# Performance work log

Measured on AMD Instinct MI355X. Metric: run time of the kernel, lower is better.

## Reference

```python
import jax, jax.numpy as jnp
import numpy as np

D_MODEL = 1024
N_HEADS = 16
D_HEAD = D_MODEL // N_HEADS

def setup_inputs() -> dict:
    key = jax.random.key(0)
    k1, k2, k3 = jax.random.split(key, 3)
    x = jax.random.normal(k1, (4, 2048, D_MODEL), dtype=jnp.float32)
    # Linear weights stored as [in, out] for x @ W
    s = 1.0 / np.sqrt(D_MODEL)
    W_qkv = jax.random.uniform(k2, (D_MODEL, 3 * D_MODEL), jnp.float32, -s, s)
    W_out = jax.random.uniform(k3, (D_MODEL, D_MODEL), jnp.float32, -s, s)
    return {"x": x, "W_qkv": W_qkv, "W_out": W_out}

def reference(x, W_qkv, W_out):
    B, T, C = x.shape
    scale = D_HEAD ** -0.5
    qkv = x @ W_qkv                       # [B,T,3C]
    q, k, v = jnp.split(qkv, 3, axis=-1)
    def heads(t):
        return t.reshape(B, T, N_HEADS, D_HEAD).transpose(0, 2, 1, 3)  # [B,H,T,d]
    q, k, v = heads(q), heads(k), heads(v)
    att = jnp.einsum('bhqd,bhkd->bhqk', q, k) * scale  # [B,H,T,T]
    causal = jnp.tril(jnp.ones((T, T), dtype=bool))
    att = jnp.where(causal, att, -jnp.inf)
    att = jax.nn.softmax(att, axis=-1)
    y = jnp.einsum('bhqk,bhkd->bhqd', att, v)          # [B,H,T,d]
    y = y.transpose(0, 2, 1, 3).reshape(B, T, C)
    return y @ W_out
```

## Files before the change

### kernel.cpp

```cpp
#include <hip/hip_runtime.h>
#include <hip/hip_bf16.h>

typedef unsigned short u16;
typedef __attribute__((ext_vector_type(8))) short short8v;
typedef __attribute__((ext_vector_type(4))) float f32x4;
typedef __attribute__((ext_vector_type(16))) float f32x16;

#define Bb 4
#define Tt 2048
#define Cc 1024
#define Hh 16
#define C3 3072
#define Mm 8192

__device__ __forceinline__ u16 f2bf(float f) {
    union { __hip_bfloat16 h; u16 u; } r;
    r.h = __float2bfloat16(f);
    return r.u;
}
__device__ __forceinline__ unsigned int pk2(float a, float b) {
    union { __hip_bfloat162 h; unsigned int u; } r;
    r.h.x = __float2bfloat16(a);
    r.h.y = __float2bfloat16(b);
    return r.u;
}
__device__ __forceinline__ float exp2g(float x) {
#if __has_builtin(__builtin_amdgcn_exp2f)
    return __builtin_amdgcn_exp2f(x);
#else
    return exp2f(x);
#endif
}
__device__ __forceinline__ void plswap(unsigned int& a, unsigned int& b) {
#if __has_builtin(__builtin_amdgcn_permlane32_swap)
    typedef __attribute__((ext_vector_type(2))) unsigned int uint2v;
    uint2v r = __builtin_amdgcn_permlane32_swap(a, b, false, false);
    a = r.x; b = r.y;
#else
    asm volatile("v_permlane32_swap_b32 %0, %1" : "+v"(a), "+v"(b));
#endif
}
__device__ __forceinline__ void gload16(const void* g, void* l) {
    __builtin_amdgcn_global_load_lds(
        (const __attribute__((address_space(1))) unsigned int*)g,
        (__attribute__((address_space(3))) unsigned int*)l, 16, 0, 0);
}

__global__ __launch_bounds__(256) void cvt_x(const float* __restrict__ in,
                                             u16* __restrict__ out) {
    int i = blockIdx.x * 256 + threadIdx.x;
    float4 v = reinterpret_cast<const float4*>(in)[i];
    ushort4 o;
    o.x = f2bf(v.x); o.y = f2bf(v.y); o.z = f2bf(v.z); o.w = f2bf(v.w);
    reinterpret_cast<ushort4*>(out)[i] = o;
}

__global__ __launch_bounds__(256) void wtrans(const float* __restrict__ in,
                                              u16* __restrict__ out,
                                              int R, int Ccols) {
    __shared__ float t[32][33];
    const int tx = threadIdx.x & 31, ty = threadIdx.x >> 5;
    const int bx = blockIdx.x, by = blockIdx.y;
    const int c = bx * 32 + tx;
#pragma unroll
    for (int j = 0; j < 4; ++j) {
        int r = by * 32 + ty + j * 8;
        t[ty + j * 8][tx] = in[(size_t)r * Ccols + c];
    }
    __syncthreads();
#pragma unroll
    for (int j = 0; j < 4; ++j) {
        int orow = bx * 32 + ty + j * 8;
        int oc   = by * 32 + tx;
        out[(size_t)orow * R + oc] = f2bf(t[tx][ty + j * 8]);
    }
}

template <int OUTF32>
__global__ __launch_bounds__(256) void gemm_mfma(const u16* __restrict__ A,
                                                 const u16* __restrict__ BT,
                                                 void* __restrict__ C0,
                                                 int M, int N, int K) {
    __shared__ u16 As[128 * 32];
    __shared__ u16 Bs[128 * 32];
    const int tid = threadIdx.x;
    const int w = tid >> 6, l = tid & 63;
    const int wr = w >> 1, wc = w & 1;
    const int g = l >> 4, q = l & 15;
    const int bm = blockIdx.x * 128, bn = blockIdx.y * 128;
    const int lrow = l >> 2;
    const int lcol = (l & 3) * 8;

    f32x4 acc[4][4] = {};
    const u16* Ap = A + (size_t)(bm + w * 32 + lrow) * K + lcol;
    const u16* Bp = BT + (size_t)(bn + w * 32 + lrow) * K + lcol;

    for (int k0 = 0; k0 < K; k0 += 32) {
        gload16(Ap + k0, &As[(w * 32) * 32]);
        gload16(Ap + (size_t)16 * K + k0, &As[(w * 32 + 16) * 32]);
        gload16(Bp + k0, &Bs[(w * 32) * 32]);
        gload16(Bp + (size_t)16 * K + k0, &Bs[(w * 32 + 16) * 32]);
        __syncthreads();
        short8v af[4], bf[4];
#pragma unroll
        for (int m = 0; m < 4; ++m)
            af[m] = *reinterpret_cast<const short8v*>(&As[(wr * 64 + m * 16 + q) * 32 + g * 8]);
#pragma unroll
        for (int n = 0; n < 4; ++n)
            bf[n] = *reinterpret_cast<const short8v*>(&Bs[(wc * 64 + n * 16 + q) * 32 + g * 8]);
#pragma unroll
        for (int m = 0; m < 4; ++m)
#pragma unroll
            for (int n = 0; n < 4; ++n)
                acc[m][n] = __builtin_amdgcn_mfma_f32_16x16x32_bf16(af[m], bf[n], acc[m][n], 0, 0, 0);
        __syncthreads();
    }

#pragma unroll
    for (int m = 0; m < 4; ++m)
#pragma unroll
        for (int n = 0; n < 4; ++n)
#pragma unroll
            for (int r = 0; r < 4; ++r) {
                int row = bm + wr * 64 + m * 16 + g * 4 + r;
                int col = bn + wc * 64 + n * 16 + q;
                if (OUTF32)
                    reinterpret_cast<float*>(C0)[(size_t)row * N + col] = acc[m][n][r];
                else
                    reinterpret_cast<u16*>(C0)[(size_t)row * N + col] = f2bf(acc[m][n][r]);
            }
}

__global__ __launch_bounds__(512, 2) void gemm256_qkv(const u16* __restrict__ A,
                                                      const u16* __restrict__ BT,
                                                      u16* __restrict__ qkOut,
                                                      u16* __restrict__ vTOut,
                                                      int K) {
    __shared__ u16 SM[65536];
    const int tid = threadIdx.x;
    const int wv = tid >> 6, L = tid & 63;
    const int wm = wv >> 2, wn = wv & 3;
    const int q = L & 15, g = L >> 4;
    const int bm = blockIdx.x * 256, bn = blockIdx.y * 256;
    const int nK = K >> 6;

    char* smB = (char*)SM;
    const int srow = wv * 16 + (L >> 3);
    const int scol = ((L & 7) ^ ((L >> 3) & 7)) * 8;
    const u16* Asrc = A + (size_t)(bm + srow) * K + scol;
    const u16* Bsrc = BT + (size_t)(bn + srow) * K + scol;

#define STG2(src, ldsByte)                                                \
    { gload16((src), smB + (ldsByte) + wv * 2048);                        \
      gload16((src) + 8 * (size_t)K, smB + (ldsByte) + wv * 2048 + 1024); }

    STG2(Asrc, 0)
    STG2(Asrc + 128 * (size_t)K, 16384)
    STG2(Bsrc, 32768)
    STG2(Bsrc + 128 * (size_t)K, 49152)
    STG2(Asrc + 64, 65536)
    STG2(Asrc + 128 * (size_t)K + 64, 65536 + 16384)
    STG2(Bsrc + 64, 65536 + 32768)

    const int rA = (wm * 128 + q) * 64;
    const int rB = 16384 + (wn * 64 + q) * 64;
    const int s0 = (g ^ (q & 7)) * 8;
    const int s1 = ((4 + g) ^ (q & 7)) * 8;

    f32x4 acc[8][4] = {};

#define MMA(mf, nf)                                                                              \
    acc[mf][nf] = __builtin_amdgcn_mfma_f32_16x16x32_bf16(Af##mf[0], Bf##nf[0], acc[mf][nf], 0, 0, 0); \
    acc[mf][nf] = __builtin_amdgcn_mfma_f32_16x16x32_bf16(Af##mf[1], Bf##nf[1], acc[mf][nf], 0, 0, 0);
#define MBLK(a, b)                                                        \
    __builtin_amdgcn_s_setprio(1);                                        \
    MMA(a, 0) MMA(a, 1) MMA(a, 2) MMA(a, 3)                               \
    MMA(b, 0) MMA(b, 1) MMA(b, 2) MMA(b, 3)                               \
    __builtin_amdgcn_s_setprio(0);

    for (int t = 0; t < nK; ++t) {
        const int bufU = (t & 1) * 32768;
        const int curB = (t & 1) * 65536;
        const int nxtB = ((t + 1) & 1) * 65536;
        if (t == nK - 1) { asm volatile("s_waitcnt vmcnt(0)" ::: "memory"); }
        else             { asm volatile("s_waitcnt vmcnt(6)" ::: "memory"); }
        __builtin_amdgcn_s_barrier();
        __builtin_amdgcn_sched_barrier(0);

        short8v Af0[2], Af1[2], Af2[2], Af3[2], Af4[2], Af5[2], Af6[2], Af7[2];
        short8v Bf0[2], Bf1[2], Bf2[2], Bf3[2];
#define LDA(mf)                                                                         \
        Af##mf[0] = *reinterpret_cast<const short8v*>(&SM[bufU + rA + mf * 1024 + s0]); \
        Af##mf[1] = *reinterpret_cast<const short8v*>(&SM[bufU + rA + mf * 1024 + s1]);
#define LDB(nf)                                                                         \
        Bf##nf[0] = *reinterpret_cast<const short8v*>(&SM[bufU + rB + nf * 1024 + s0]); \
        Bf##nf[1] = *reinterpret_cast<const short8v*>(&SM[bufU + rB + nf * 1024 + s1]);
        LDA(0) LDA(1) LDA(2) LDA(3) LDA(4) LDA(5) LDA(6) LDA(7)
        LDB(0) LDB(1) LDB(2) LDB(3)
#undef LDA
#undef LDB
        asm volatile("s_waitcnt lgkmcnt(0)" ::: "memory");
        __builtin_amdgcn_sched_barrier(0);
        __builtin_amdgcn_s_barrier();

        if (t + 1 < nK) STG2(Bsrc + 128 * (size_t)K + (t + 1) * 64, nxtB + 49152)
        MBLK(0, 1)
        if (t + 2 < nK) STG2(Asrc + (t + 2) * 64, curB)
        MBLK(2, 3)
        if (t + 2 < nK) STG2(Asrc + 128 * (size_t)K + (t + 2) * 64, curB + 16384)
        MBLK(4, 5)
        if (t + 2 < nK) STG2(Bsrc + (t + 2) * 64, curB + 32768)
        MBLK(6, 7)
    }
#undef MMA
#undef MBLK
#undef STG2

#pragma unroll
    for (int mf = 0; mf < 8; ++mf)
#pragma unroll
        for (int nf = 0; nf < 4; ++nf) {
            const int col = bn + wn * 64 + nf * 16 + q;
#pragma unroll
            for (int rr = 0; rr < 4; ++rr) {
                const int row = bm + wm * 128 + mf * 16 + g * 4 + rr;
                const u16 v = f2bf(acc[mf][nf][rr]);
                if (col < 2048) {
                    qkOut[(size_t)row * 2048 + col] = v;
                } else {
                    const int bI = row >> 11, tI = row & 2047;
                    vTOut[((size_t)bI * 1024 + (col - 2048)) * 2048 + tI] = v;
                }
            }
        }
}

__global__ __launch_bounds__(256) void attn_mfma(const u16* __restrict__ qk,
                                                 const u16* __restrict__ vT,
                                                 u16* __restrict__ y) {
    __shared__ u16 SM[18432];
    const int tid = threadIdx.x;
    const int w = tid >> 6, l = tid & 63;
    const int q31 = l & 31, hi = l >> 5;
    const int bid = blockIdx.x;
    const int bh = bid & 63, c0 = bid >> 6;
    const int b = bh >> 4, h = bh & 15;
    const size_t tok0 = (size_t)b * Tt;

    const float C2 = 0.18033688011112042f;
    const float THR = 44.361419555836499f;

    const int srow = tid >> 2;
    const int sseg = (tid & 3) * 16;
    const int soff = srow * 72 + sseg;
    const u16* gK = qk + (tok0 + srow) * 2048 + 1024 + h * 64 + sseg;
    const u16* gV = vT + ((size_t)b * 1024 + h * 64 + srow) * 2048 + sseg;

    for (int phase = 0; phase < 2; ++phase) {
        const int chunk = phase ? (15 - c0) : c0;
        const int nsteps = 2 * (chunk + 1);
        const int q0w = chunk * 128 + w * 32;
        const int qlane = q0w + q31;

        short8v qf0, qf1, qf2, qf3;
        {
            const u16* qp = qk + (tok0 + qlane) * 2048 + h * 64 + hi * 8;
            qf0 = *reinterpret_cast<const short8v*>(qp);
            qf1 = *reinterpret_cast<const short8v*>(qp + 16);
            qf2 = *reinterpret_cast<const short8v*>(qp + 32);
            qf3 = *reinterpret_cast<const short8v*>(qp + 48);
        }

        f32x16 acc0 = {}, acc1 = {};
        float m_run = -1e30f, l_run = 0.f;

        {
            uint4 ka = *reinterpret_cast<const uint4*>(gK);
            uint4 kb = *reinterpret_cast<const uint4*>(gK + 8);
            uint4 va = *reinterpret_cast<const uint4*>(gV);
            uint4 vb = *reinterpret_cast<const uint4*>(gV + 8);
            *reinterpret_cast<uint4*>(&SM[soff]) = ka;
            *reinterpret_cast<uint4*>(&SM[soff + 8]) = kb;
            *reinterpret_cast<uint4*>(&SM[9216 + soff]) = va;
            *reinterpret_cast<uint4*>(&SM[9216 + soff + 8]) = vb;
        }
        __syncthreads();

        for (int t = 0; t < nsteps; ++t) {
            const int cur = t & 1;
            const int k0 = t * 64;
            const bool pre = (t + 1 < nsteps);
            uint4 ka = {}, kb = {}, va = {}, vb = {};
            if (pre) {
                const u16* gKt = gK + (size_t)(t + 1) * 64 * 2048;
                const u16* gVt = gV + (t + 1) * 64;
                ka = *reinterpret_cast<const uint4*>(gKt);
                kb = *reinterpret_cast<const uint4*>(gKt + 8);
                va = *reinterpret_cast<const uint4*>(gVt);
                vb = *reinterpret_cast<const uint4*>(gVt + 8);
            }

            if (k0 <= q0w + 31) {
                const u16* Kb = SM + cur * 4608;
                const u16* Vb = SM + 9216 + cur * 4608;
                f32x16 st0 = {}, st1 = {};
#pragma unroll
                for (int s = 0; s < 4; ++s) {
                    short8v kfa = *reinterpret_cast<const short8v*>(&Kb[q31 * 72 + s * 16 + hi * 8]);
                    short8v kfb = *reinterpret_cast<const short8v*>(&Kb[(q31 + 32) * 72 + s * 16 + hi * 8]);
                    short8v qs = (s == 0) ? qf0 : (s == 1) ? qf1 : (s == 2) ? qf2 : qf3;
                    st0 = __builtin_amdgcn_mfma_f32_32x32x16_bf16(kfa, qs, st0, 0, 0, 0);
                    st1 = __builtin_amdgcn_mfma_f32_32x32x16_bf16(kfb, qs, st1, 0, 0, 0);
                }
                const bool diag = (k0 + 63 > q0w);
                float s0[16], s1[16];
                float mx = -1e30f;
#pragma unroll
                for (int r = 0; r < 16; ++r) {
                    int krel = (r & 3) + 8 * (r >> 2) + 4 * hi;
                    float v0 = st0[r];
                    float v1 = st1[r];
                    if (diag) {
                        if (k0 + krel > qlane) v0 = -1e30f;
                        if (k0 + 32 + krel > qlane) v1 = -1e30f;
                    }
                    s0[r] = v0; s1[r] = v1;
                    mx = fmaxf(mx, fmaxf(v0, v1));
                }
                mx = fmaxf(mx, __shfl_xor(mx, 32));
                if (!__all(mx <= m_run + THR)) {
                    float m_new = fmaxf(m_run, mx);
                    float alpha = exp2g((m_run - m_new) * C2);
                    l_run *= alpha;
                    acc0 *= alpha;
                    acc1 *= alpha;
                    m_run = m_new;
                }
                const float mc = m_run * C2;
                float rs = 0.f;
#pragma unroll
                for (int r = 0; r < 16; ++r) {
                    float p0 = exp2g(fmaf(s0[r], C2, -mc));
                    float p1 = exp2g(fmaf(s1[r], C2, -mc));
                    s0[r] = p0; s1[r] = p1;
                    rs += p0 + p1;
                }
                rs += __shfl_xor(rs, 32);
                l_run += rs;

                short8v pf0, pf1, pf2, pf3;
#define MKFRAG(dst, P, rb)                                                  \
                {                                                           \
                    unsigned int a_ = pk2(P[rb + 0], P[rb + 1]);            \
                    unsigned int b_ = pk2(P[rb + 4], P[rb + 5]);            \
                    unsigned int c_ = pk2(P[rb + 2], P[rb + 3]);            \
                    unsigned int d_ = pk2(P[rb + 6], P[rb + 7]);            \
                    plswap(a_, b_);                                         \
                    plswap(c_, d_);                                         \
                    union { unsigned int u[4]; short8v s; } uf_;            \
                    uf_.u[0] = a_; uf_.u[1] = c_; uf_.u[2] = b_; uf_.u[3] = d_; \
                    dst = uf_.s;                                            \
                }
                MKFRAG(pf0, s0, 0)
                MKFRAG(pf1, s0, 8)
                MKFRAG(pf2, s1, 0)
                MKFRAG(pf3, s1, 8)
#undef MKFRAG
#pragma unroll
                for (int s = 0; s < 4; ++s) {
                    short8v vfa = *reinterpret_cast<const short8v*>(&Vb[q31 * 72 + s * 16 + hi * 8]);
                    short8v vfb = *reinterpret_cast<const short8v*>(&Vb[(q31 + 32) * 72 + s * 16 + hi * 8]);
                    short8v ps = (s == 0) ? pf0 : (s == 1) ? pf1 : (s == 2) ? pf2 : pf3;
                    acc0 = __builtin_amdgcn_mfma_f32_32x32x16_bf16(vfa, ps, acc0, 0, 0, 0);
                    acc1 = __builtin_amdgcn_mfma_f32_32x32x16_bf16(vfb, ps, acc1, 0, 0, 0);
                }
            }

            if (pre) {
                const int nb = cur ^ 1;
                *reinterpret_cast<uint4*>(&SM[nb * 4608 + soff]) = ka;
                *reinterpret_cast<uint4*>(&SM[nb * 4608 + soff + 8]) = kb;
                *reinterpret_cast<uint4*>(&SM[9216 + nb * 4608 + soff]) = va;
                *reinterpret_cast<uint4*>(&SM[9216 + nb * 4608 + soff + 8]) = vb;
            }
            __syncthreads();
        }

        const float inv = 1.f / l_run;
        unsigned int* Od2 = reinterpret_cast<unsigned int*>(SM);
        const int qrow = w * 32 + q31;
#pragma unroll
        for (int r = 0; r < 16; r += 2) {
            int d0 = (r & 3) + 8 * (r >> 2) + 4 * hi;
            Od2[qrow * 36 + (d0 >> 1)] = pk2(acc0[r] * inv, acc0[r + 1] * inv);
            Od2[qrow * 36 + ((32 + d0) >> 1)] = pk2(acc1[r] * inv, acc1[r + 1] * inv);
        }
        __syncthreads();
        {
            const int row = w * 32 + (l >> 1);
            const int dh = (l & 1) * 32;
            const u16* src = SM + row * 72 + dh;
            u16* dst = y + (tok0 + chunk * 128 + row) * Cc + h * 64 + dh;
#pragma unroll
            for (int k2 = 0; k2 < 4; ++k2)
                *reinterpret_cast<uint4*>(dst + k2 * 8) =
                    *reinterpret_cast<const uint4*>(src + k2 * 8);
        }
        __syncthreads();
    }
}

extern "C" void kernel_launch(void* const* d_in, const int* in_sizes, int n_in,
                              void* d_out, int out_size, void* d_ws, size_t ws_size,
                              hipStream_t stream) {
    const float* x    = (const float*)d_in[0];
    const float* Wqkv = (const float*)d_in[1];
    const float* Wout = (const float*)d_in[2];
    float* out = (float*)d_out;

    char* ws = (char*)d_ws;
    u16* qk    = (u16*)(ws);
    u16* vT    = (u16*)(ws + 33554432);
    u16* xbf   = (u16*)(ws + 50331648);
    u16* WqkvT = (u16*)(ws + 67108864);
    u16* WoutT = (u16*)(ws + 73400320);

    cvt_x<<<(Mm * Cc) / (256 * 4), 256, 0, stream>>>(x, xbf);
    wtrans<<<dim3(C3 / 32, Cc / 32), 256, 0, stream>>>(Wqkv, WqkvT, Cc, C3);
    wtrans<<<dim3(Cc / 32, Cc / 32), 256, 0, stream>>>(Wout, WoutT, Cc, Cc);

    gemm256_qkv<<<dim3(Mm / 256, C3 / 256), 512, 0, stream>>>(xbf, WqkvT, qk, vT, Cc);

    u16* ybf = xbf;
    attn_mfma<<<512, 256, 0, stream>>>(qk, vT, ybf);

    gemm_mfma<1><<<dim3(Mm / 128, Cc / 128), 256, 0, stream>>>(ybf, WoutT, out, Mm, Cc, Cc);
}
```

Before: 214.1 us.

## Interleave LDS A-fragment loads with MFMA blocks in QKV GEMM main loop

Restructures the GEMM K-loop so A fragments are read from LDS in pairs just before their MFMA block, instead of loading all fragments up front. The goal is to overlap LDS reads with matrix-core work and lower the register count for A fragments. The three global-to-LDS stages for t+2 are grouped after the barrier instead of being spread between MFMA blocks. This risks unhidden LDS latency inside sched_barrier-fenced regions, bunched global loads, and a race if the next-stage writes land before every wave has finished reading.

```diff
diff --git a/kernel.cpp b/kernel.cpp
--- a/kernel.cpp
+++ b/kernel.cpp
@@ -169,13 +169,19 @@
 
     f32x4 acc[8][4] = {};
 
-#define MMA(mf, nf)                                                                              \
-    acc[mf][nf] = __builtin_amdgcn_mfma_f32_16x16x32_bf16(Af##mf[0], Bf##nf[0], acc[mf][nf], 0, 0, 0); \
-    acc[mf][nf] = __builtin_amdgcn_mfma_f32_16x16x32_bf16(Af##mf[1], Bf##nf[1], acc[mf][nf], 0, 0, 0);
-#define MBLK(a, b)                                                        \
+#define LDA2(dst, mf)                                                                   \
+    dst[0] = *reinterpret_cast<const short8v*>(&SM[bufU + rA + mf * 1024 + s0]);        \
+    dst[1] = *reinterpret_cast<const short8v*>(&SM[bufU + rA + mf * 1024 + s1]);
+#define LDB2(nf)                                                                        \
+    Bf##nf[0] = *reinterpret_cast<const short8v*>(&SM[bufU + rB + nf * 1024 + s0]);     \
+    Bf##nf[1] = *reinterpret_cast<const short8v*>(&SM[bufU + rB + nf * 1024 + s1]);
+#define MMA2(Aa, nf, ia)                                                                       \
+    acc[ia][nf] = __builtin_amdgcn_mfma_f32_16x16x32_bf16(Aa[0], Bf##nf[0], acc[ia][nf], 0, 0, 0); \
+    acc[ia][nf] = __builtin_amdgcn_mfma_f32_16x16x32_bf16(Aa[1], Bf##nf[1], acc[ia][nf], 0, 0, 0);
+#define MBLK2(Aa, Ab, ia, ib)                                             \
     __builtin_amdgcn_s_setprio(1);                                        \
-    MMA(a, 0) MMA(a, 1) MMA(a, 2) MMA(a, 3)                               \
-    MMA(b, 0) MMA(b, 1) MMA(b, 2) MMA(b, 3)                               \
+    MMA2(Aa, 0, ia) MMA2(Aa, 1, ia) MMA2(Aa, 2, ia) MMA2(Aa, 3, ia)       \
+    MMA2(Ab, 0, ib) MMA2(Ab, 1, ib) MMA2(Ab, 2, ib) MMA2(Ab, 3, ib)       \
     __builtin_amdgcn_s_setprio(0);
 
     for (int t = 0; t < nK; ++t) {
@@ -187,33 +193,44 @@
         __builtin_amdgcn_s_barrier();
         __builtin_amdgcn_sched_barrier(0);
 
-        short8v Af0[2], Af1[2], Af2[2], Af3[2], Af4[2], Af5[2], Af6[2], Af7[2];
         short8v Bf0[2], Bf1[2], Bf2[2], Bf3[2];
-#define LDA(mf)                                                                         \
-        Af##mf[0] = *reinterpret_cast<const short8v*>(&SM[bufU + rA + mf * 1024 + s0]); \
-        Af##mf[1] = *reinterpret_cast<const short8v*>(&SM[bufU + rA + mf * 1024 + s1]);
-#define LDB(nf)                                                                         \
-        Bf##nf[0] = *reinterpret_cast<const short8v*>(&SM[bufU + rB + nf * 1024 + s0]); \
-        Bf##nf[1] = *reinterpret_cast<const short8v*>(&SM[bufU + rB + nf * 1024 + s1]);
-        LDA(0) LDA(1) LDA(2) LDA(3) LDA(4) LDA(5) LDA(6) LDA(7)
-        LDB(0) LDB(1) LDB(2) LDB(3)
-#undef LDA
-#undef LDB
+        LDB2(0) LDB2(1) LDB2(2) LDB2(3)
+        short8v Af0[2], Af1[2];
+        LDA2(Af0, 0) LDA2(Af1, 1)
+        if (t + 1 < nK) STG2(Bsrc + 128 * (size_t)K + (t + 1) * 64, nxtB + 49152)
+        __builtin_amdgcn_sched_barrier(0);
+        MBLK2(Af0, Af1, 0, 1)
+        __builtin_amdgcn_sched_barrier(0);
+
+        short8v Af2[2], Af3[2];
+        LDA2(Af2, 2) LDA2(Af3, 3)
+        __builtin_amdgcn_sched_barrier(0);
+        MBLK2(Af2, Af3, 2, 3)
+        __builtin_amdgcn_sched_barrier(0);
+
+        short8v Af4[2], Af5[2];
+        LDA2(Af4, 4) LDA2(Af5, 5)
+        __builtin_amdgcn_sched_barrier(0);
+        MBLK2(Af4, Af5, 4, 5)
+        __builtin_amdgcn_sched_barrier(0);
+
+        short8v Af6[2], Af7[2];
+        LDA2(Af6, 6) LDA2(Af7, 7)
         asm volatile("s_waitcnt lgkmcnt(0)" ::: "memory");
         __builtin_amdgcn_sched_barrier(0);
         __builtin_amdgcn_s_barrier();
-
-        if (t + 1 < nK) STG2(Bsrc + 128 * (size_t)K + (t + 1) * 64, nxtB + 49152)
-        MBLK(0, 1)
-        if (t + 2 < nK) STG2(Asrc + (t + 2) * 64, curB)
-        MBLK(2, 3)
-        if (t + 2 < nK) STG2(Asrc + 128 * (size_t)K + (t + 2) * 64, curB + 16384)
-        MBLK(4, 5)
-        if (t + 2 < nK) STG2(Bsrc + (t + 2) * 64, curB + 32768)
-        MBLK(6, 7)
+        if (t + 2 < nK) {
+            STG2(Asrc + (t + 2) * 64, curB)
+            STG2(Asrc + 128 * (size_t)K + (t + 2) * 64, curB + 16384)
+            STG2(Bsrc + (t + 2) * 64, curB + 32768)
+        }
+        __builtin_amdgcn_sched_barrier(0);
+        MBLK2(Af6, Af7, 6, 7)
     }
-#undef MMA
-#undef MBLK
+#undef MMA2
+#undef MBLK2
+#undef LDA2
+#undef LDB2
 #undef STG2
 
 #pragma unroll
```

Result: no change. 211.0 us (-1.5%).
